# Kernel tuning notes

Measured on AMD Instinct MI355X. Metric: run time of the kernel, lower is better.

## Reference

```python
import jax, jax.numpy as jnp
import numpy as np

NUM_HEADER = 8
DIM_HIDDEN = 512
DIM_HEADER = DIM_HIDDEN // NUM_HEADER


def setup_inputs() -> dict:
    key = jax.random.key(0)
    ks = jax.random.split(key, 11)
    B, S, D = 2, 4096, DIM_HIDDEN
    scale = 1.0 / np.sqrt(D)
    inp = {
        "q": jax.random.normal(ks[0], (B, S, D), jnp.float32),
        "k": jax.random.normal(ks[1], (B, S, D), jnp.float32),
        "v": jax.random.normal(ks[2], (B, S, D), jnp.float32),
        # nn.Linear weights are [out, in]; y = x @ W.T + b
        "Wq": jax.random.normal(ks[3], (D, D), jnp.float32) * scale,
        "bq": jax.random.normal(ks[4], (D,), jnp.float32) * scale,
        "Wk": jax.random.normal(ks[5], (D, D), jnp.float32) * scale,
        "bk": jax.random.normal(ks[6], (D,), jnp.float32) * scale,
        "Wv": jax.random.normal(ks[7], (D, D), jnp.float32) * scale,
        "bv": jax.random.normal(ks[8], (D,), jnp.float32) * scale,
        "Wo": jax.random.normal(ks[9], (D, D), jnp.float32) * scale,
        "bo": jax.random.normal(ks[10], (D,), jnp.float32) * scale,
    }
    return inp


def reference(q, k, v, Wq, bq, Wk, bk, Wv, bv, Wo, bo):
    B = q.shape[0]
    H, dh = NUM_HEADER, DIM_HEADER

    def proj(x, W, b):
        # [B,S,D] -> [B,H,S,dh]
        y = jnp.einsum('bsd,ed->bse', x, W) + b
        return y.reshape(B, -1, H, dh).transpose(0, 2, 1, 3)

    qh = proj(q, Wq, bq)
    kh = proj(k, Wk, bk)
    vh = proj(v, Wv, bv)

    scores = jnp.einsum('bhqd,bhkd->bhqk', qh, kh) / jnp.sqrt(jnp.float32(dh))
    attn = jax.nn.softmax(scores, axis=-1)
    ctx = jnp.einsum('bhqk,bhkd->bhqd', attn, vh)
    concat = ctx.transpose(0, 2, 1, 3).reshape(B, -1, H * dh)
    return jnp.einsum('bsd,ed->bse', concat, Wo) + bo
```

## Files before the change

### kernel.cpp

```cpp
#include <hip/hip_runtime.h>
#include <hip/hip_bf16.h>

typedef __attribute__((ext_vector_type(8))) short short8;
typedef __attribute__((ext_vector_type(4))) float f32x4;
typedef __attribute__((ext_vector_type(16))) float f32x16;
typedef __attribute__((ext_vector_type(4))) float f4v;

#define SEQ 4096
#define NBH 16
#define SCALE_Q 0.18033688011112042f

#define MFMA16(a, b, c) __builtin_amdgcn_mfma_f32_16x16x32_bf16(a, b, c, 0, 0, 0)
#define MFMA32(a, b, c) __builtin_amdgcn_mfma_f32_32x32x16_bf16(a, b, c, 0, 0, 0)

__device__ __forceinline__ short f2bf(float f) {
  union { float f; unsigned u; } x; x.f = f;
  unsigned r = x.u + 0x7FFFu + ((x.u >> 16) & 1u);
  return (short)(r >> 16);
}

__device__ __forceinline__ float bf2f(short s) {
  union { unsigned u; float f; } x;
  x.u = ((unsigned)(unsigned short)s) << 16;
  return x.f;
}

__device__ __forceinline__ unsigned cvt_pk_bf16(float lo, float hi) {
  unsigned r;
  asm("v_cvt_pk_bf16_f32 %0, %1, %2" : "=v"(r) : "v"(lo), "v"(hi));
  return r;
}

__device__ __forceinline__ short8 cvt8(const float* __restrict__ src) {
  f4v v0 = *(const f4v*)src;
  f4v v1 = *(const f4v*)(src + 4);
  union { unsigned u[4]; short8 s; } r;
  r.u[0] = cvt_pk_bf16(v0[0], v0[1]);
  r.u[1] = cvt_pk_bf16(v0[2], v0[3]);
  r.u[2] = cvt_pk_bf16(v1[0], v1[1]);
  r.u[3] = cvt_pk_bf16(v1[2], v1[3]);
  return r.s;
}

__device__ __forceinline__ void gll16(const void* g, void* l) {
  __builtin_amdgcn_global_load_lds(
      (const __attribute__((address_space(1))) void*)g,
      (__attribute__((address_space(3))) void*)l, 16, 0, 0);
}

__device__ __forceinline__ void pswap(unsigned& a, unsigned& b) {
  asm volatile("v_permlane32_swap_b32 %0, %1" : "+v"(a), "+v"(b));
}

#define SBAR()                              \
  __builtin_amdgcn_sched_barrier(0);        \
  __builtin_amdgcn_s_barrier();             \
  __builtin_amdgcn_sched_barrier(0)

__global__ __launch_bounds__(256) void cvt_w(
    const float* __restrict__ w0, const float* __restrict__ w1,
    const float* __restrict__ w2, const float* __restrict__ w3,
    short* __restrict__ dst)
{
  int i = blockIdx.x * 256 + threadIdx.x;
  int m = i >> 15;
  int off = (i & 32767) * 8;
  const float* s = (m == 0) ? w0 : (m == 1) ? w1 : (m == 2) ? w2 : w3;
  *(short8*)(dst + (size_t)m * 262144 + off) = cvt8(s + off);
}

template <bool SWAP>
__device__ __forceinline__ void qkv_kloop(
    const float* __restrict__ Af, const short* __restrict__ W,
    char* smemA, char* smemB, f32x4 (&acc)[4][2],
    int tile_m, int tile_n, int t, int g, int q, int w)
{
  short (*As)[72] = (short(*)[72])smemA;
  for (int k0 = 0; k0 < 512; k0 += 64) {
    __syncthreads();
#pragma unroll
    for (int it = 0; it < 2; ++it) {
      int i = it * 256 + t;
      int r = i >> 3, sg = i & 7;
      *(short8*)&As[r][sg * 8] =
          cvt8(Af + (size_t)(tile_m + r) * 512 + k0 + sg * 8);
    }
#pragma unroll
    for (int it = 0; it < 4; ++it) {
      int i = it * 256 + t;
      int row = i >> 3, cg = i & 7;
      const char* gp = (const char*)W +
          ((size_t)(tile_n + row) * 512 + k0) * 2 + ((cg ^ (row & 7)) << 4);
      gll16(gp, smemB + (size_t)(it * 256 + (t & ~63)) * 16);
    }
    __syncthreads();
#pragma unroll
    for (int kk = 0; kk < 2; ++kk) {
      short8 af[4], bfv[2];
#pragma unroll
      for (int mi = 0; mi < 4; ++mi)
        af[mi] = *(const short8*)&As[mi * 16 + q][kk * 32 + g * 8];
#pragma unroll
      for (int ni = 0; ni < 2; ++ni) {
        int rB = w * 32 + ni * 16 + q;
        bfv[ni] = *(const short8*)(smemB + rB * 128 +
                                   (((4 * kk + g) ^ (rB & 7)) << 4));
      }
#pragma unroll
      for (int mi = 0; mi < 4; ++mi)
#pragma unroll
        for (int ni = 0; ni < 2; ++ni) {
          if (SWAP)
            acc[mi][ni] = MFMA16(bfv[ni], af[mi], acc[mi][ni]);
          else
            acc[mi][ni] = MFMA16(af[mi], bfv[ni], acc[mi][ni]);
        }
    }
  }
}

__global__ __launch_bounds__(256) void qkv_gemm(
    const float* __restrict__ qin, const float* __restrict__ kin,
    const float* __restrict__ vin, const short* __restrict__ Wb,
    const float* __restrict__ bq, const float* __restrict__ bk,
    const float* __restrict__ bv,
    short* __restrict__ Qh, short* __restrict__ Kh, short* __restrict__ Vt)
{
  __shared__ __align__(16) char smemA[64 * 72 * 2];
  __shared__ __align__(16) char smemB[128 * 64 * 2];
  const int t    = threadIdx.x;
  const int lane = t & 63;
  const int w    = t >> 6;
  const int g    = lane >> 4;
  const int q    = lane & 15;
  const int tile_n = blockIdx.x * 128;
  const int tile_m = blockIdx.y * 64;
  const int z      = blockIdx.z;

  const float* Af   = (z == 0) ? qin : (z == 1) ? kin : vin;
  const float* bias = (z == 0) ? bq  : (z == 1) ? bk  : bv;
  const short* W    = Wb + (size_t)z * 262144;

  f32x4 acc[4][2];
#pragma unroll
  for (int mi = 0; mi < 4; ++mi)
#pragma unroll
    for (int ni = 0; ni < 2; ++ni)
#pragma unroll
      for (int j = 0; j < 4; ++j) acc[mi][ni][j] = 0.f;

  if (z == 2)
    qkv_kloop<true>(Af, W, smemA, smemB, acc, tile_m, tile_n, t, g, q, w);
  else
    qkv_kloop<false>(Af, W, smemA, smemB, acc, tile_m, tile_n, t, g, q, w);

#pragma unroll
  for (int mi = 0; mi < 4; ++mi) {
#pragma unroll
    for (int ni = 0; ni < 2; ++ni) {
#pragma unroll
      for (int j = 0; j < 4; ++j) {
        if (z == 2) {
          int e = tile_n + w * 32 + ni * 16 + 4 * g + j;
          int srow = tile_m + mi * 16 + q;
          float val = acc[mi][ni][j] + bias[e];
          int b = srow >> 12, sl = srow & 4095;
          int h = e >> 6, d = e & 63;
          Vt[((size_t)((b * 8 + h) * 64 + d)) * SEQ + sl] = f2bf(val);
        } else {
          int m = tile_m + mi * 16 + g * 4 + j;
          int e = tile_n + w * 32 + ni * 16 + q;
          float val = acc[mi][ni][j] + bias[e];
          int b = m >> 12, s = m & 4095;
          int h = e >> 6, d = e & 63;
          size_t off = ((size_t)(b * 8 + h) * SEQ + s) * 64 + d;
          if (z == 0) Qh[off] = f2bf(val * SCALE_Q);
          else        Kh[off] = f2bf(val);
        }
      }
    }
  }
}

template <int MODE>
__global__ __launch_bounds__(256) void gemm_bt(
    const short* __restrict__ Ab,
    const short* __restrict__ Wb, const float* __restrict__ bias,
    const short* __restrict__ OpartB, const float* __restrict__ lsum,
    void* __restrict__ Cout)
{
  __shared__ __align__(16) char smemA[64 * 72 * 2];
  __shared__ __align__(16) char smemB[128 * 64 * 2];
  const int t    = threadIdx.x;
  const int lane = t & 63;
  const int w    = t >> 6;
  const int g    = lane >> 4;
  const int q    = lane & 15;
  const int tile_n = blockIdx.x * 128;
  const int tile_m = blockIdx.y * 64;

  f32x4 acc[4][2];
#pragma unroll
  for (int mi = 0; mi < 4; ++mi)
#pragma unroll
    for (int ni = 0; ni < 2; ++ni)
#pragma unroll
      for (int j = 0; j < 4; ++j) acc[mi][ni][j] = 0.f;

  for (int k0 = 0; k0 < 512; k0 += 64) {
    __syncthreads();
    if (MODE == 3) {
#pragma unroll
      for (int it = 0; it < 2; ++it) {
        int i = it * 256 + t;
        int row = i >> 3, cg = i & 7;
        const char* gp = (const char*)Ab +
            ((size_t)(tile_m + row) * 512 + k0) * 2 + ((cg ^ (row & 7)) << 4);
        gll16(gp, smemA + (size_t)(it * 256 + (t & ~63)) * 16);
      }
    } else {
#pragma unroll
      for (int it = 0; it < 2; ++it) {
        int i = it * 256 + t;
        int row = i >> 3, cg = i & 7;
        int cgs = cg ^ (row & 7);
        int m = tile_m + row;
        int b = m >> 12, s = m & 4095;
        int h = k0 >> 6;
        size_t base = (size_t)(b * 8 + h) * SEQ + s;
        float ltot = 0.f;
#pragma unroll
        for (int sp = 0; sp < 4; ++sp)
          ltot += lsum[base + (size_t)sp * NBH * SEQ];
        float inv = 1.0f / ltot;
        float vv[8];
#pragma unroll
        for (int j = 0; j < 8; ++j) vv[j] = 0.f;
#pragma unroll
        for (int sp = 0; sp < 4; ++sp) {
          short8 o = *(const short8*)(OpartB +
              (base + (size_t)sp * NBH * SEQ) * 64 + cgs * 8);
#pragma unroll
          for (int j = 0; j < 8; ++j) vv[j] += bf2f(o[j]);
        }
#pragma unroll
        for (int j = 0; j < 8; ++j) vv[j] *= inv;
        union { unsigned u[4]; short8 s8; } r;
        r.u[0] = cvt_pk_bf16(vv[0], vv[1]);
        r.u[1] = cvt_pk_bf16(vv[2], vv[3]);
        r.u[2] = cvt_pk_bf16(vv[4], vv[5]);
        r.u[3] = cvt_pk_bf16(vv[6], vv[7]);
        *(short8*)(smemA + (size_t)i * 16) = r.s8;
      }
    }
#pragma unroll
    for (int it = 0; it < 4; ++it) {
      int i = it * 256 + t;
      int row = i >> 3, cg = i & 7;
      const char* gp = (const char*)Wb +
          ((size_t)(tile_n + row) * 512 + k0) * 2 + ((cg ^ (row & 7)) << 4);
      gll16(gp, smemB + (size_t)(it * 256 + (t & ~63)) * 16);
    }
    __syncthreads();
#pragma unroll
    for (int kk = 0; kk < 2; ++kk) {
      short8 af[4], bfv[2];
#pragma unroll
      for (int mi = 0; mi < 4; ++mi) {
        int rA = mi * 16 + q;
        af[mi] = *(const short8*)(smemA + rA * 128 +
                                  (((4 * kk + g) ^ (rA & 7)) << 4));
      }
#pragma unroll
      for (int ni = 0; ni < 2; ++ni) {
        int rB = w * 32 + ni * 16 + q;
        bfv[ni] = *(const short8*)(smemB + rB * 128 +
                                   (((4 * kk + g) ^ (rB & 7)) << 4));
      }
#pragma unroll
      for (int mi = 0; mi < 4; ++mi)
#pragma unroll
        for (int ni = 0; ni < 2; ++ni)
          acc[mi][ni] = MFMA16(af[mi], bfv[ni], acc[mi][ni]);
    }
  }

#pragma unroll
  for (int mi = 0; mi < 4; ++mi) {
#pragma unroll
    for (int ni = 0; ni < 2; ++ni) {
#pragma unroll
      for (int j = 0; j < 4; ++j) {
        int m = tile_m + mi * 16 + g * 4 + j;
        int e = tile_n + w * 32 + ni * 16 + q;
        ((float*)Cout)[(size_t)m * 512 + e] = acc[mi][ni][j] + bias[e];
      }
    }
  }
}

template <int NSPLIT>
__global__ __launch_bounds__(512, 4) void attn_kernel(
    const short* __restrict__ Qh, const short* __restrict__ Kh,
    const short* __restrict__ Vt, short* __restrict__ ctx,
    short* __restrict__ OpartB, float* __restrict__ lsum)
{
  __shared__ __align__(16) char smem[2][8192];
  const int t    = threadIdx.x;
  const int lane = t & 63;
  const int w    = t >> 6;
  const int l31  = lane & 31;
  const int hi   = lane >> 5;

  const int fid = blockIdx.x;
  int qt, bh, split;
  if (NSPLIT == 1) {
    int lid = (fid & 7) * 32 + (fid >> 3);
    qt = lid & 15; bh = lid >> 4; split = 0;
  } else {
    int lid = (fid & 7) * 128 + (fid >> 3);
    qt = lid & 15; split = (lid >> 4) & 3; bh = lid >> 6;
  }
  const int NT  = (SEQ / 32) / NSPLIT;
  const int kt0 = split * NT;

  const size_t kbase = (size_t)bh * SEQ * 64;
  const size_t vbase = (size_t)bh * 64 * SEQ;
  const int q0 = qt * 256 + w * 32;

  short8 qf[4];
#pragma unroll
  for (int m = 0; m < 4; ++m)
    qf[m] = *(const short8*)(Qh + kbase + (size_t)(q0 + l31) * 64 + m * 16 + hi * 8);

  f32x16 fz;
#pragma unroll
  for (int r = 0; r < 16; ++r) fz[r] = 0.f;
  f32x16 acc0 = fz, acc1 = fz;
  float lrun = 0.f;

  const int rif   = lane >> 3;
  const int scolK = ((lane & 7) ^ rif) * 16;
  const int svcol = ((lane & 3) ^ ((lane >> 3) & 3)) * 16;
  const int xr    = (hi * 16) ^ ((lane & 7) << 4);
  const int xrv   = (hi * 16) ^ (((l31 >> 1) & 3) << 4);

#define STAGE(buf, kt)                                                         \
  {                                                                            \
    int c = w;                                                                 \
    char* ldst = &smem[buf][c * 1024];                                         \
    if (c < 4) {                                                               \
      int row = c * 8 + rif;                                                   \
      const char* gp = (const char*)Kh +                                       \
          ((kbase + (size_t)((kt) * 32 + row) * 64) * 2 + scolK);              \
      gll16(gp, ldst);                                                         \
    } else {                                                                   \
      int row = (c - 4) * 16 + (lane >> 2);                                    \
      const char* gp = (const char*)Vt +                                       \
          ((vbase + (size_t)row * SEQ + (kt) * 32) * 2 + svcol);               \
      gll16(gp, ldst);                                                         \
    }                                                                          \
  }

  STAGE(0, kt0);
  int cur = 0;

  for (int it = 0; it < NT; ++it) {
    const int kt = kt0 + it;
    asm volatile("s_waitcnt vmcnt(0)" ::: "memory");
    SBAR();
    if (it < NT - 1) STAGE(cur ^ 1, kt + 1);

    const char* Kb = &smem[cur][0];
    const char* Vb = &smem[cur][4096];

    f32x16 s0;
    {
      short8 k0 = *(const short8*)(Kb + (size_t)(l31) * 128 + ((32 * 0) ^ xr));
      __builtin_amdgcn_s_setprio(1);
      s0 = MFMA32(k0, qf[0], fz);
      __builtin_amdgcn_s_setprio(0);
    }
#pragma unroll
    for (int m = 1; m < 4; ++m) {
      short8 k0 = *(const short8*)(Kb + (size_t)(l31) * 128 + ((32 * m) ^ xr));
      __builtin_amdgcn_s_setprio(1);
      s0 = MFMA32(k0, qf[m], s0);
      __builtin_amdgcn_s_setprio(0);
    }

#pragma unroll
    for (int r = 0; r < 16; ++r) s0[r] = __builtin_amdgcn_exp2f(s0[r]);
    float rs;
    {
      float b_[8];
#pragma unroll
      for (int r = 0; r < 8; ++r) b_[r] = s0[r] + s0[r + 8];
#pragma unroll
      for (int r = 0; r < 4; ++r) b_[r] += b_[r + 4];
      rs = (b_[0] + b_[1]) + (b_[2] + b_[3]);
    }
    rs += __shfl_xor(rs, 32);
    lrun += rs;

    union { unsigned u[4]; short8 v; } A0c, A1c;
    {
      unsigned p0 = cvt_pk_bf16(s0[0], s0[1]);
      unsigned p1 = cvt_pk_bf16(s0[2], s0[3]);
      unsigned p2 = cvt_pk_bf16(s0[4], s0[5]);
      unsigned p3 = cvt_pk_bf16(s0[6], s0[7]);
      unsigned p4 = cvt_pk_bf16(s0[8], s0[9]);
      unsigned p5 = cvt_pk_bf16(s0[10], s0[11]);
      unsigned p6 = cvt_pk_bf16(s0[12], s0[13]);
      unsigned p7 = cvt_pk_bf16(s0[14], s0[15]);
      pswap(p0, p2); pswap(p1, p3); pswap(p4, p6); pswap(p5, p7);
      A0c.u[0] = p0; A0c.u[1] = p1; A0c.u[2] = p2; A0c.u[3] = p3;
      A1c.u[0] = p4; A1c.u[1] = p5; A1c.u[2] = p6; A1c.u[3] = p7;
    }

#pragma unroll
    for (int h2 = 0; h2 < 2; ++h2) {
      short8 pa = h2 ? A1c.v : A0c.v;
      short8 vf0 = *(const short8*)(Vb + (size_t)(l31) * 64 + ((32 * h2) ^ xrv));
      short8 vf1 = *(const short8*)(Vb + (size_t)(32 + l31) * 64 + ((32 * h2) ^ xrv));
      __builtin_amdgcn_s_setprio(1);
      acc0 = MFMA32(pa, vf0, acc0);
      acc1 = MFMA32(pa, vf1, acc1);
      __builtin_amdgcn_s_setprio(0);
    }

    cur ^= 1;
  }

  if (NSPLIT == 1) {
    const int b = bh >> 3, hh = bh & 7;
    const float inv = 1.0f / lrun;
#pragma unroll
    for (int r = 0; r < 16; ++r) {
      int ql = (r & 3) + 8 * (r >> 2) + 4 * hi;
      float iv = __shfl(inv, ql);
      int qrow = q0 + ql;
      size_t off = ((size_t)(b * SEQ + qrow)) * 512 + hh * 64 + l31;
      ctx[off]      = f2bf(acc0[r] * iv);
      ctx[off + 32] = f2bf(acc1[r] * iv);
    }
  } else {
    short* Ob = OpartB + ((size_t)(split * NBH + bh) * SEQ + q0) * 64;
#pragma unroll
    for (int r = 0; r < 16; ++r) {
      int ql = (r & 3) + 8 * (r >> 2) + 4 * hi;
      Ob[(size_t)ql * 64 + l31]      = f2bf(acc0[r]);
      Ob[(size_t)ql * 64 + l31 + 32] = f2bf(acc1[r]);
    }
    if (hi == 0)
      lsum[(size_t)(split * NBH + bh) * SEQ + q0 + l31] = lrun;
  }
}

extern "C" void kernel_launch(void* const* d_in, const int* in_sizes, int n_in,
                              void* d_out, int out_size, void* d_ws, size_t ws_size,
                              hipStream_t stream) {
  const float* q  = (const float*)d_in[0];
  const float* k  = (const float*)d_in[1];
  const float* v  = (const float*)d_in[2];
  const float* Wq = (const float*)d_in[3];
  const float* bq = (const float*)d_in[4];
  const float* Wk = (const float*)d_in[5];
  const float* bk = (const float*)d_in[6];
  const float* Wv = (const float*)d_in[7];
  const float* bv = (const float*)d_in[8];
  const float* Wo = (const float*)d_in[9];
  const float* bo = (const float*)d_in[10];

  const size_t NELT = (size_t)NBH * SEQ * 64;
  short* Qh  = (short*)d_ws;
  short* Kh  = Qh + NELT;
  short* Vt  = Kh + NELT;
  short* ctx    = Vt + NELT;
  short* OpartB = ctx;
  short* Wb     = OpartB + 4 * NELT;
  float* lsum   = (float*)(Wb + 4 * 262144);
  const char* ws_end = (const char*)(lsum + 4 * (size_t)NBH * SEQ);
  const bool split4 = ws_size >= (size_t)(ws_end - (const char*)d_ws);

  dim3 tb(256);
  cvt_w<<<dim3(512), tb, 0, stream>>>(Wq, Wk, Wv, Wo, Wb);

  qkv_gemm<<<dim3(4, 128, 3), tb, 0, stream>>>(q, k, v, Wb, bq, bk, bv,
                                               Qh, Kh, Vt);
  if (split4) {
    attn_kernel<4><<<dim3(1024), dim3(512), 0, stream>>>(Qh, Kh, Vt, ctx, OpartB, lsum);
    gemm_bt<4><<<dim3(4, 128), tb, 0, stream>>>(nullptr, Wb + 786432, bo, OpartB, lsum, d_out);
  } else {
    attn_kernel<1><<<dim3(256), dim3(512), 0, stream>>>(Qh, Kh, Vt, ctx, OpartB, lsum);
    gemm_bt<3><<<dim3(4, 128), tb, 0, stream>>>(ctx, Wb + 786432, bo, nullptr, nullptr, d_out);
  }
}
```

Measured before the change: 160.8 us.

## Process two 32-row query tiles per wave to reuse staged K/V fragments

After: 160.0 us (median of 2 runs). No clear change (-0.6%).

```diff
diff --git a/kernel.cpp b/kernel.cpp
--- a/kernel.cpp
+++ b/kernel.cpp
@@ -300,7 +300,7 @@
 }
 
 template <int NSPLIT>
-__global__ __launch_bounds__(512, 4) void attn_kernel(
+__global__ __launch_bounds__(512, 2) void attn_kernel(
     const short* __restrict__ Qh, const short* __restrict__ Kh,
     const short* __restrict__ Vt, short* __restrict__ ctx,
     short* __restrict__ OpartB, float* __restrict__ lsum)
@@ -315,29 +315,31 @@
   const int fid = blockIdx.x;
   int qt, bh, split;
   if (NSPLIT == 1) {
-    int lid = (fid & 7) * 32 + (fid >> 3);
-    qt = lid & 15; bh = lid >> 4; split = 0;
+    int lid = (fid & 7) * 16 + (fid >> 3);
+    qt = lid & 7; bh = lid >> 3; split = 0;
   } else {
-    int lid = (fid & 7) * 128 + (fid >> 3);
-    qt = lid & 15; split = (lid >> 4) & 3; bh = lid >> 6;
+    int lid = (fid & 7) * 64 + (fid >> 3);
+    qt = lid & 7; split = (lid >> 3) & 3; bh = lid >> 5;
   }
   const int NT  = (SEQ / 32) / NSPLIT;
   const int kt0 = split * NT;
 
   const size_t kbase = (size_t)bh * SEQ * 64;
   const size_t vbase = (size_t)bh * 64 * SEQ;
-  const int q0 = qt * 256 + w * 32;
-
-  short8 qf[4];
-#pragma unroll
-  for (int m = 0; m < 4; ++m)
-    qf[m] = *(const short8*)(Qh + kbase + (size_t)(q0 + l31) * 64 + m * 16 + hi * 8);
+  const int q0 = qt * 512 + w * 64;
+
+  short8 qfA[4], qfB[4];
+#pragma unroll
+  for (int m = 0; m < 4; ++m) {
+    qfA[m] = *(const short8*)(Qh + kbase + (size_t)(q0 + l31) * 64 + m * 16 + hi * 8);
+    qfB[m] = *(const short8*)(Qh + kbase + (size_t)(q0 + 32 + l31) * 64 + m * 16 + hi * 8);
+  }
 
   f32x16 fz;
 #pragma unroll
   for (int r = 0; r < 16; ++r) fz[r] = 0.f;
-  f32x16 acc0 = fz, acc1 = fz;
-  float lrun = 0.f;
+  f32x16 accA0 = fz, accA1 = fz, accB0 = fz, accB1 = fz;
+  float lrunA = 0.f, lrunB = 0.f;
 
   const int rif   = lane >> 3;
   const int scolK = ((lane & 7) ^ rif) * 16;
@@ -374,58 +376,89 @@
     const char* Kb = &smem[cur][0];
     const char* Vb = &smem[cur][4096];
 
-    f32x16 s0;
+    f32x16 sa, sb;
     {
       short8 k0 = *(const short8*)(Kb + (size_t)(l31) * 128 + ((32 * 0) ^ xr));
       __builtin_amdgcn_s_setprio(1);
-      s0 = MFMA32(k0, qf[0], fz);
+      sa = MFMA32(k0, qfA[0], fz);
+      sb = MFMA32(k0, qfB[0], fz);
       __builtin_amdgcn_s_setprio(0);
     }
 #pragma unroll
     for (int m = 1; m < 4; ++m) {
       short8 k0 = *(const short8*)(Kb + (size_t)(l31) * 128 + ((32 * m) ^ xr));
       __builtin_amdgcn_s_setprio(1);
-      s0 = MFMA32(k0, qf[m], s0);
+      sa = MFMA32(k0, qfA[m], sa);
+      sb = MFMA32(k0, qfB[m], sb);
       __builtin_amdgcn_s_setprio(0);
     }
 
 #pragma unroll
-    for (int r = 0; r < 16; ++r) s0[r] = __builtin_amdgcn_exp2f(s0[r]);
-    float rs;
+    for (int r = 0; r < 16; ++r) sa[r] = __builtin_amdgcn_exp2f(sa[r]);
+    float rsA;
     {
       float b_[8];
 #pragma unroll
-      for (int r = 0; r < 8; ++r) b_[r] = s0[r] + s0[r + 8];
+      for (int r = 0; r < 8; ++r) b_[r] = sa[r] + sa[r + 8];
 #pragma unroll
       for (int r = 0; r < 4; ++r) b_[r] += b_[r + 4];
-      rs = (b_[0] + b_[1]) + (b_[2] + b_[3]);
-    }
-    rs += __shfl_xor(rs, 32);
-    lrun += rs;
-
-    union { unsigned u[4]; short8 v; } A0c, A1c;
+      rsA = (b_[0] + b_[1]) + (b_[2] + b_[3]);
+    }
+    rsA += __shfl_xor(rsA, 32);
+    lrunA += rsA;
+    union { unsigned u[4]; short8 v; } A0a, A1a, A0b, A1b;
     {
-      unsigned p0 = cvt_pk_bf16(s0[0], s0[1]);
-      unsigned p1 = cvt_pk_bf16(s0[2], s0[3]);
-      unsigned p2 = cvt_pk_bf16(s0[4], s0[5]);
-      unsigned p3 = cvt_pk_bf16(s0[6], s0[7]);
-      unsigned p4 = cvt_pk_bf16(s0[8], s0[9]);
-      unsigned p5 = cvt_pk_bf16(s0[10], s0[11]);
-      unsigned p6 = cvt_pk_bf16(s0[12], s0[13]);
-      unsigned p7 = cvt_pk_bf16(s0[14], s0[15]);
+      unsigned p0 = cvt_pk_bf16(sa[0], sa[1]);
+      unsigned p1 = cvt_pk_bf16(sa[2], sa[3]);
+      unsigned p2 = cvt_pk_bf16(sa[4], sa[5]);
+      unsigned p3 = cvt_pk_bf16(sa[6], sa[7]);
+      unsigned p4 = cvt_pk_bf16(sa[8], sa[9]);
+      unsigned p5 = cvt_pk_bf16(sa[10], sa[11]);
+      unsigned p6 = cvt_pk_bf16(sa[12], sa[13]);
+      unsigned p7 = cvt_pk_bf16(sa[14], sa[15]);
       pswap(p0, p2); pswap(p1, p3); pswap(p4, p6); pswap(p5, p7);
-      A0c.u[0] = p0; A0c.u[1] = p1; A0c.u[2] = p2; A0c.u[3] = p3;
-      A1c.u[0] = p4; A1c.u[1] = p5; A1c.u[2] = p6; A1c.u[3] = p7;
+      A0a.u[0] = p0; A0a.u[1] = p1; A0a.u[2] = p2; A0a.u[3] = p3;
+      A1a.u[0] = p4; A1a.u[1] = p5; A1a.u[2] = p6; A1a.u[3] = p7;
+    }
+
+#pragma unroll
+    for (int r = 0; r < 16; ++r) sb[r] = __builtin_amdgcn_exp2f(sb[r]);
+    float rsB;
+    {
+      float b_[8];
+#pragma unroll
+      for (int r = 0; r < 8; ++r) b_[r] = sb[r] + sb[r + 8];
+#pragma unroll
+      for (int r = 0; r < 4; ++r) b_[r] += b_[r + 4];
+      rsB = (b_[0] + b_[1]) + (b_[2] + b_[3]);
+    }
+    rsB += __shfl_xor(rsB, 32);
+    lrunB += rsB;
+    {
+      unsigned p0 = cvt_pk_bf16(sb[0], sb[1]);
+      unsigned p1 = cvt_pk_bf16(sb[2], sb[3]);
+      unsigned p2 = cvt_pk_bf16(sb[4], sb[5]);
+      unsigned p3 = cvt_pk_bf16(sb[6], sb[7]);
+      unsigned p4 = cvt_pk_bf16(sb[8], sb[9]);
+      unsigned p5 = cvt_pk_bf16(sb[10], sb[11]);
+      unsigned p6 = cvt_pk_bf16(sb[12], sb[13]);
+      unsigned p7 = cvt_pk_bf16(sb[14], sb[15]);
+      pswap(p0, p2); pswap(p1, p3); pswap(p4, p6); pswap(p5, p7);
+      A0b.u[0] = p0; A0b.u[1] = p1; A0b.u[2] = p2; A0b.u[3] = p3;
+      A1b.u[0] = p4; A1b.u[1] = p5; A1b.u[2] = p6; A1b.u[3] = p7;
     }
 
 #pragma unroll
     for (int h2 = 0; h2 < 2; ++h2) {
-      short8 pa = h2 ? A1c.v : A0c.v;
+      short8 paA = h2 ? A1a.v : A0a.v;
+      short8 paB = h2 ? A1b.v : A0b.v;
       short8 vf0 = *(const short8*)(Vb + (size_t)(l31) * 64 + ((32 * h2) ^ xrv));
       short8 vf1 = *(const short8*)(Vb + (size_t)(32 + l31) * 64 + ((32 * h2) ^ xrv));
       __builtin_amdgcn_s_setprio(1);
-      acc0 = MFMA32(pa, vf0, acc0);
-      acc1 = MFMA32(pa, vf1, acc1);
+      accA0 = MFMA32(paA, vf0, accA0);
+      accB0 = MFMA32(paB, vf0, accB0);
+      accA1 = MFMA32(paA, vf1, accA1);
+      accB1 = MFMA32(paB, vf1, accB1);
       __builtin_amdgcn_s_setprio(0);
     }
 
@@ -434,26 +467,34 @@
 
   if (NSPLIT == 1) {
     const int b = bh >> 3, hh = bh & 7;
-    const float inv = 1.0f / lrun;
+    const float invA = 1.0f / lrunA;
+    const float invB = 1.0f / lrunB;
 #pragma unroll
     for (int r = 0; r < 16; ++r) {
       int ql = (r & 3) + 8 * (r >> 2) + 4 * hi;
-      float iv = __shfl(inv, ql);
-      int qrow = q0 + ql;
-      size_t off = ((size_t)(b * SEQ + qrow)) * 512 + hh * 64 + l31;
-      ctx[off]      = f2bf(acc0[r] * iv);
-      ctx[off + 32] = f2bf(acc1[r] * iv);
+      float ivA = __shfl(invA, ql);
+      float ivB = __shfl(invB, ql);
+      size_t offA = ((size_t)(b * SEQ + q0 + ql)) * 512 + hh * 64 + l31;
+      size_t offB = ((size_t)(b * SEQ + q0 + 32 + ql)) * 512 + hh * 64 + l31;
+      ctx[offA]      = f2bf(accA0[r] * ivA);
+      ctx[offA + 32] = f2bf(accA1[r] * ivA);
+      ctx[offB]      = f2bf(accB0[r] * ivB);
+      ctx[offB + 32] = f2bf(accB1[r] * ivB);
     }
   } else {
     short* Ob = OpartB + ((size_t)(split * NBH + bh) * SEQ + q0) * 64;
 #pragma unroll
     for (int r = 0; r < 16; ++r) {
       int ql = (r & 3) + 8 * (r >> 2) + 4 * hi;
-      Ob[(size_t)ql * 64 + l31]      = f2bf(acc0[r]);
-      Ob[(size_t)ql * 64 + l31 + 32] = f2bf(acc1[r]);
-    }
-    if (hi == 0)
-      lsum[(size_t)(split * NBH + bh) * SEQ + q0 + l31] = lrun;
+      Ob[(size_t)ql * 64 + l31]             = f2bf(accA0[r]);
+      Ob[(size_t)ql * 64 + l31 + 32]        = f2bf(accA1[r]);
+      Ob[(size_t)(32 + ql) * 64 + l31]      = f2bf(accB0[r]);
+      Ob[(size_t)(32 + ql) * 64 + l31 + 32] = f2bf(accB1[r]);
+    }
+    if (hi == 0) {
+      lsum[(size_t)(split * NBH + bh) * SEQ + q0 + l31]      = lrunA;
+      lsum[(size_t)(split * NBH + bh) * SEQ + q0 + 32 + l31] = lrunB;
+    }
   }
 }
 
@@ -489,10 +530,10 @@
   qkv_gemm<<<dim3(4, 128, 3), tb, 0, stream>>>(q, k, v, Wb, bq, bk, bv,
                                                Qh, Kh, Vt);
   if (split4) {
-    attn_kernel<4><<<dim3(1024), dim3(512), 0, stream>>>(Qh, Kh, Vt, ctx, OpartB, lsum);
+    attn_kernel<4><<<dim3(512), dim3(512), 0, stream>>>(Qh, Kh, Vt, ctx, OpartB, lsum);
     gemm_bt<4><<<dim3(4, 128), tb, 0, stream>>>(nullptr, Wb + 786432, bo, OpartB, lsum, d_out);
   } else {
-    attn_kernel<1><<<dim3(256), dim3(512), 0, stream>>>(Qh, Kh, Vt, ctx, OpartB, lsum);
+    attn_kernel<1><<<dim3(128), dim3(512), 0, stream>>>(Qh, Kh, Vt, ctx, OpartB, lsum);
     gemm_bt<3><<<dim3(4, 128), tb, 0, stream>>>(ctx, Wb + 786432, bo, nullptr, nullptr, d_out);
   }
 }
```
